# Optimization experiments

Hardware: AMD Instinct MI355X
Metric: run time of the kernel (lower is better)

Reference implementation:

```python
import jax, jax.numpy as jnp
import numpy as np

C = 768
H = 12
HD = C // H  # 64


def setup_inputs() -> dict:
    key = jax.random.key(0)
    k1, k2, k3, k4, k5, k6 = jax.random.split(key, 6)
    B, T = 8, 1024
    x = jax.random.normal(k1, (B, T, C), dtype=jnp.float32)
    mask = jax.random.randint(k2, (B, T), 0, 2, dtype=jnp.int32)
    # Linear params stored so that y = x @ W + b (W is [in, out])
    W_attn = jax.random.normal(k3, (C, 3 * C), dtype=jnp.float32) * 0.02
    b_attn = jax.random.normal(k4, (3 * C,), dtype=jnp.float32) * 0.02
    W_proj = jax.random.normal(k5, (C, C), dtype=jnp.float32) * 0.02
    b_proj = jax.random.normal(k6, (C,), dtype=jnp.float32) * 0.02
    return {"x": x, "mask": mask, "W_attn": W_attn, "b_attn": b_attn,
            "W_proj": W_proj, "b_proj": b_proj}


def reference(x, mask, W_attn, b_attn, W_proj, b_proj):
    B, T, _ = x.shape
    qkv = x @ W_attn + b_attn                      # [B, T, 3C]
    q, k, v = jnp.split(qkv, 3, axis=2)            # each [B, T, C]
    # [B, T, C] -> [B, H, T, HD]
    q = q.reshape(B, T, H, HD).transpose(0, 2, 1, 3)
    k = k.reshape(B, T, H, HD).transpose(0, 2, 1, 3)
    v = v.reshape(B, T, H, HD).transpose(0, 2, 1, 3)

    scale = 1.0 / np.sqrt(HD).astype(np.float32)
    att = jnp.einsum('bhqd,bhkd->bhqk', q, k) * scale  # [B, H, T, T]

    causal = jnp.tril(jnp.ones((T, T), dtype=bool))    # [T, T]
    att = jnp.where(causal[None, None], att, -jnp.inf)

    # custom mask: per-(batch, query-row) flag; where mask==0 the whole row
    # of scores is overwritten with 0.0001 (AFTER causal fill, as in torch)
    row_masked = (mask == 0)[:, None, :, None]         # [B, 1, T, 1]
    att = jnp.where(row_masked, jnp.float32(1e-4), att)

    att = jax.nn.softmax(att, axis=-1)
    # dropout layers are identity in eval mode
    y = jnp.einsum('bhqk,bhkd->bhqd', att, v)          # [B, H, T, HD]
    y = y.transpose(0, 2, 1, 3).reshape(B, T, C)
    y = y @ W_proj + b_proj
    return y
```

## Files before the change

kernel.cpp:

```cpp
#include <hip/hip_runtime.h>

#define BQ 8
#define TT 1024
#define CC 768
#define NH 12
#define HD 64
#define BH (BQ*NH)
#define MROWS (BQ*TT)
#define NQKV (3*CC)
#define KD CC

typedef unsigned short u16;
typedef __attribute__((ext_vector_type(4))) short short4v;
typedef __attribute__((ext_vector_type(8))) short short8v;
typedef __attribute__((ext_vector_type(4))) float floatx4;
typedef __attribute__((address_space(1))) const unsigned int gu32;
typedef __attribute__((address_space(3))) unsigned int lu32;

__device__ __forceinline__ float bf2f(u16 u) {
  union { unsigned int i; float f; } c; c.i = ((unsigned int)u) << 16; return c.f;
}
__device__ __forceinline__ u16 f2bf(float f) {
  union { float f; unsigned int i; } c; c.f = f;
  unsigned int i = c.i;
  return (u16)((i + 0x7FFFu + ((i >> 16) & 1u)) >> 16);
}
__device__ __forceinline__ float fast_exp2(float x) {
  return __builtin_amdgcn_exp2f(x);
}
__device__ __forceinline__ void async_ld16(const u16* g, u16* l) {
  __builtin_amdgcn_global_load_lds((gu32*)g, (lu32*)l, 16, 0, 0);
}

__global__ __launch_bounds__(256) void convert_f32_bf16(
    const float* __restrict__ in, u16* __restrict__ out, int n)
{
  int i = (blockIdx.x * 256 + threadIdx.x) * 4;
  if (i >= n) return;
  floatx4 v = *(const floatx4*)(in + i);
  short4v o;
  o[0] = (short)f2bf(v[0]); o[1] = (short)f2bf(v[1]);
  o[2] = (short)f2bf(v[2]); o[3] = (short)f2bf(v[3]);
  *(short4v*)(out + i) = o;
}

__global__ __launch_bounds__(256) void transpose_f32_bf16(
    const float* __restrict__ in, u16* __restrict__ out, int R, int Cc)
{
  __shared__ float tile[32][33];
  int ct = Cc >> 5;
  int bx = blockIdx.x % ct;
  int by = blockIdx.x / ct;
  int tx = threadIdx.x & 31;
  int ty = threadIdx.x >> 5;
  int c0 = bx << 5, r0 = by << 5;
#pragma unroll
  for (int s = 0; s < 4; ++s)
    tile[ty + s*8][tx] = in[(size_t)(r0 + ty + s*8) * Cc + c0 + tx];
  __syncthreads();
#pragma unroll
  for (int s = 0; s < 4; ++s)
    out[(size_t)(c0 + ty + s*8) * R + r0 + tx] = f2bf(tile[tx][ty + s*8]);
}

__global__ __launch_bounds__(256) void gemm_bt(
    const u16* __restrict__ A, const u16* __restrict__ Bt,
    const float* __restrict__ bias,
    float* __restrict__ out,
    u16* __restrict__ qo, u16* __restrict__ ko, u16* __restrict__ vo,
    int M, int N, int mode)
{
  __shared__ u16 As[64 * 64];
  __shared__ u16 Bs[128 * 64];

  int tid = threadIdx.x;
  int lane = tid & 63;
  int w = tid >> 6;
  int c = lane & 15;
  int q4 = lane >> 4;

  int mtiles = M >> 6;
  int mt = blockIdx.x % mtiles;
  int nt = blockIdx.x / mtiles;
  int m0 = mt << 6, n0 = nt << 7;

  int wr = (w >> 1) << 5;
  int wc = (w & 1) << 6;

  int srow8 = lane >> 3;
  int ug = ((lane & 7) ^ srow8) << 3;
  const u16* ag = A  + (size_t)(m0 + w * 16 + srow8) * KD + ug;
  const u16* bg = Bt + (size_t)(n0 + w * 32 + srow8) * KD + ug;
  u16* asl = &As[(w * 16) * 64];
  u16* bsl = &Bs[(w * 32) * 64];

  floatx4 acc[2][4];
#pragma unroll
  for (int mi = 0; mi < 2; ++mi)
#pragma unroll
    for (int ni = 0; ni < 4; ++ni) acc[mi][ni] = (floatx4){0.f, 0.f, 0.f, 0.f};

  int c7 = c & 7;

#pragma unroll 1
  for (int kt = 0; kt < KD; kt += 64) {
    async_ld16(ag + kt,              asl);
    async_ld16(ag + kt + 8 * KD,     asl + 8 * 64);
    async_ld16(bg + kt,              bsl);
    async_ld16(bg + kt + 8 * KD,     bsl + 8 * 64);
    async_ld16(bg + kt + 16 * KD,    bsl + 16 * 64);
    async_ld16(bg + kt + 24 * KD,    bsl + 24 * 64);
    __syncthreads();

    short8v af[2][2], bf[4][2];
#pragma unroll
    for (int kc = 0; kc < 2; ++kc) {
      int uoff = ((kc * 4 + q4) ^ c7) << 3;
#pragma unroll
      for (int mi = 0; mi < 2; ++mi)
        af[mi][kc] = *(const short8v*)&As[(wr + mi * 16 + c) * 64 + uoff];
#pragma unroll
      for (int ni = 0; ni < 4; ++ni)
        bf[ni][kc] = *(const short8v*)&Bs[(wc + ni * 16 + c) * 64 + uoff];
    }
#pragma unroll
    for (int kc = 0; kc < 2; ++kc)
#pragma unroll
      for (int mi = 0; mi < 2; ++mi)
#pragma unroll
        for (int ni = 0; ni < 4; ++ni)
          acc[mi][ni] = __builtin_amdgcn_mfma_f32_16x16x32_bf16(af[mi][kc], bf[ni][kc], acc[mi][ni], 0, 0, 0);
    __syncthreads();
  }

  if (mode == 0) {
    int which = (n0 + wc) / CC;
    int nbase = (n0 + wc) - which * CC;
    u16* dst0 = (which == 0) ? qo : ((which == 1) ? ko : vo);
#pragma unroll
    for (int ni = 0; ni < 4; ++ni) {
      int nn = nbase + ni * 16 + c;
      int hh = nn >> 6, dd = nn & 63;
      float bv = bias[which * CC + nn];
#pragma unroll
      for (int mi = 0; mi < 2; ++mi) {
#pragma unroll
        for (int r = 0; r < 4; ++r) {
          int mm = m0 + wr + mi * 16 + q4 * 4 + r;
          int bb = mm >> 10, tt = mm & 1023;
          size_t idx = (((size_t)(bb * NH + hh)) * TT + tt) * HD + dd;
          dst0[idx] = f2bf(acc[mi][ni][r] + bv);
        }
      }
    }
  } else {
#pragma unroll
    for (int ni = 0; ni < 4; ++ni) {
      int nn = n0 + wc + ni * 16 + c;
      float bv = bias[nn];
#pragma unroll
      for (int mi = 0; mi < 2; ++mi) {
#pragma unroll
        for (int r = 0; r < 4; ++r) {
          int mm = m0 + wr + mi * 16 + q4 * 4 + r;
          out[(size_t)mm * N + nn] = acc[mi][ni][r] + bv;
        }
      }
    }
  }
}

__global__ __launch_bounds__(256) void transpose_v(
    const u16* __restrict__ vb, u16* __restrict__ vt)
{
  __shared__ u16 tile[64][72];
  int tid = threadIdx.x;
  int tt0 = (blockIdx.x & 15) << 6;
  int bh = blockIdx.x >> 4;
  {
    int trow = tid >> 2;
    int dchunk = (tid & 3) << 4;
    const u16* src = vb + (((size_t)bh * TT + tt0 + trow) * HD) + dchunk;
    *(short8v*)&tile[trow][dchunk]     = *(const short8v*)src;
    *(short8v*)&tile[trow][dchunk + 8] = *(const short8v*)(src + 8);
  }
  __syncthreads();
  {
    int drow = tid >> 2;
    int tchunk = (tid & 3) << 4;
    short8v a, bv;
#pragma unroll
    for (int j = 0; j < 8; ++j) {
      a[j]  = (short)tile[tchunk + j][drow];
      bv[j] = (short)tile[tchunk + 8 + j][drow];
    }
    u16* dst = vt + ((size_t)bh * HD + drow) * TT + tt0 + tchunk;
    *(short8v*)dst       = a;
    *(short8v*)(dst + 8) = bv;
  }
}

__global__ __launch_bounds__(64) void vmean_kernel(
    const u16* __restrict__ vb, float* __restrict__ mv)
{
  int bh = blockIdx.x;
  int d = threadIdx.x;
  const u16* p = vb + (size_t)bh * TT * HD + d;
  float s0 = 0.f, s1 = 0.f, s2 = 0.f, s3 = 0.f;
  for (int t = 0; t < TT; t += 4) {
    s0 += bf2f(p[(size_t)(t + 0) * HD]);
    s1 += bf2f(p[(size_t)(t + 1) * HD]);
    s2 += bf2f(p[(size_t)(t + 2) * HD]);
    s3 += bf2f(p[(size_t)(t + 3) * HD]);
  }
  mv[bh * HD + d] = (s0 + s1 + s2 + s3) * (1.0f / 1024.0f);
}

__global__ __launch_bounds__(256) void knorm_kernel(
    const u16* __restrict__ kb, float* __restrict__ kmaxn)
{
  __shared__ float red[256];
  int bh = blockIdx.x;
  int tid = threadIdx.x;
  float mx = 0.f;
#pragma unroll 1
  for (int t = tid; t < TT; t += 256) {
    const u16* p = kb + ((size_t)bh * TT + t) * HD;
    float s = 0.f;
#pragma unroll
    for (int j = 0; j < 64; j += 8) {
      short8v v = *(const short8v*)(p + j);
#pragma unroll
      for (int i = 0; i < 8; ++i) {
        float f = bf2f((u16)v[i]);
        s = fmaf(f, f, s);
      }
    }
    mx = fmaxf(mx, s);
  }
  red[tid] = mx;
  __syncthreads();
  for (int s2 = 128; s2 > 0; s2 >>= 1) {
    if (tid < s2) red[tid] = fmaxf(red[tid], red[tid + s2]);
    __syncthreads();
  }
  if (tid == 0) kmaxn[bh] = sqrtf(red[0]);
}

#define LDW 72
#define SCL 0.18033688f

__global__ __launch_bounds__(256) void attn_kernel(
    const u16* __restrict__ qb, const u16* __restrict__ kb,
    const u16* __restrict__ vtb, const int* __restrict__ mask,
    const float* __restrict__ meanv, const float* __restrict__ kmaxn,
    u16* __restrict__ outb)
{
  __shared__ u16 Ks[64 * LDW];
  __shared__ u16 Vs[64 * LDW];
  __shared__ u16 Ps[4][16 * LDW];

  int tid = threadIdx.x;
  int lane = tid & 63;
  int w = tid >> 6;
  int c = lane & 15;
  int q4 = lane >> 4;

  int pair = blockIdx.x & 7;
  int bh = blockIdx.x >> 3;
  int b = bh / NH;
  int h = bh - b * NH;
  float kmax = kmaxn[bh];

  int srow = tid >> 2;
  int schunk = (tid & 3) << 4;
  const u16* kgp = kb + ((size_t)bh * TT + srow) * HD + schunk;
  const u16* vgp = vtb + ((size_t)bh * HD + srow) * TT + schunk;
  u16* ksw = &Ks[srow * LDW + schunk];
  u16* vsw = &Vs[srow * LDW + schunk];
  u16* pw = &Ps[w][0];

  short8v onesv;
#pragma unroll
  for (int j = 0; j < 8; ++j) onesv[j] = (short)0x3F80;

#pragma unroll 1
  for (int phase = 0; phase < 2; ++phase) {
    int qt = phase ? (15 - pair) : pair;
    int rowbase = (qt << 6) + (w << 4);

    short8v qfrag[2];
    {
      const u16* qp = qb + ((size_t)bh * TT + rowbase + c) * HD + q4 * 8;
      qfrag[0] = *(const short8v*)qp;
      qfrag[1] = *(const short8v*)(qp + 32);
    }

    float q2 = 0.f;
#pragma unroll
    for (int kc = 0; kc < 2; ++kc)
#pragma unroll
      for (int j = 0; j < 8; ++j) {
        float qv = bf2f((u16)qfrag[kc][j]);
        q2 = fmaf(qv, qv, q2);
      }
    q2 += __shfl_xor(q2, 16);
    q2 += __shfl_xor(q2, 32);
    float Mc = sqrtf(q2) * kmax * SCL;
    float Mrow[4];
#pragma unroll
    for (int r = 0; r < 4; ++r) Mrow[r] = __shfl(Mc, (q4 << 2) + r);

    floatx4 o[4];
#pragma unroll
    for (int i = 0; i < 4; ++i) o[i] = (floatx4){0.f, 0.f, 0.f, 0.f};
    floatx4 o5 = (floatx4){0.f, 0.f, 0.f, 0.f};

    short8v kr0, kr1, vr0, vr1;
    kr0 = *(const short8v*)kgp;
    kr1 = *(const short8v*)(kgp + 8);
    vr0 = *(const short8v*)vgp;
    vr1 = *(const short8v*)(vgp + 8);

#pragma unroll 1
    for (int kt = 0; kt <= qt; ++kt) {
      __syncthreads();
      *(short8v*)ksw = kr0; *(short8v*)(ksw + 8) = kr1;
      *(short8v*)vsw = vr0; *(short8v*)(vsw + 8) = vr1;
      __syncthreads();

      if (kt < qt) {
        const u16* kp = kgp + ((size_t)(kt + 1) << 6) * HD;
        const u16* vp = vgp + ((kt + 1) << 6);
        kr0 = *(const short8v*)kp;
        kr1 = *(const short8v*)(kp + 8);
        vr0 = *(const short8v*)vp;
        vr1 = *(const short8v*)(vp + 8);
      }

      floatx4 s[4];
#pragma unroll
      for (int nt = 0; nt < 4; ++nt) s[nt] = (floatx4){0.f, 0.f, 0.f, 0.f};
#pragma unroll
      for (int kc = 0; kc < 2; ++kc) {
#pragma unroll
        for (int nt = 0; nt < 4; ++nt) {
          short8v kf = *(const short8v*)&Ks[(nt * 16 + c) * LDW + kc * 32 + q4 * 8];
          s[nt] = __builtin_amdgcn_mfma_f32_16x16x32_bf16(qfrag[kc], kf, s[nt], 0, 0, 0);
        }
      }

      if (kt == qt) {
#pragma unroll
        for (int nt = 0; nt < 4; ++nt)
#pragma unroll
          for (int r = 0; r < 4; ++r) {
            float sv = s[nt][r];
            if (nt * 16 + c > (w << 4) + q4 * 4 + r) sv = -INFINITY;
            float p = fast_exp2(fmaf(sv, SCL, -Mrow[r]));
            pw[(q4 * 4 + r) * LDW + nt * 16 + c] = f2bf(p);
          }
      } else {
#pragma unroll
        for (int nt = 0; nt < 4; ++nt)
#pragma unroll
          for (int r = 0; r < 4; ++r) {
            float p = fast_exp2(fmaf(s[nt][r], SCL, -Mrow[r]));
            pw[(q4 * 4 + r) * LDW + nt * 16 + c] = f2bf(p);
          }
      }

#pragma unroll
      for (int kc = 0; kc < 2; ++kc) {
        short8v pf = *(const short8v*)&pw[c * LDW + kc * 32 + q4 * 8];
#pragma unroll
        for (int nt = 0; nt < 4; ++nt) {
          short8v vf = *(const short8v*)&Vs[(nt * 16 + c) * LDW + kc * 32 + q4 * 8];
          o[nt] = __builtin_amdgcn_mfma_f32_16x16x32_bf16(pf, vf, o[nt], 0, 0, 0);
        }
        o5 = __builtin_amdgcn_mfma_f32_16x16x32_bf16(pf, onesv, o5, 0, 0, 0);
      }
    }

    int qrow[4]; bool msk[4]; float inv[4];
#pragma unroll
    for (int r = 0; r < 4; ++r) {
      qrow[r] = rowbase + q4 * 4 + r;
      msk[r] = (mask[b * TT + qrow[r]] == 0);
      inv[r] = 1.f / o5[r];
    }
#pragma unroll
    for (int nt = 0; nt < 4; ++nt) {
      int d = nt * 16 + c;
      float mv = meanv[bh * HD + d];
#pragma unroll
      for (int r = 0; r < 4; ++r) {
        float val = msk[r] ? mv : o[nt][r] * inv[r];
        outb[((size_t)(b * TT + qrow[r])) * CC + h * HD + d] = f2bf(val);
      }
    }
  }
}

extern "C" void kernel_launch(void* const* d_in, const int* in_sizes, int n_in,
                              void* d_out, int out_size, void* d_ws, size_t ws_size,
                              hipStream_t stream)
{
  (void)in_sizes; (void)n_in; (void)out_size; (void)ws_size;
  const float* x     = (const float*)d_in[0];
  const int*   mask  = (const int*)d_in[1];
  const float* Wattn = (const float*)d_in[2];
  const float* battn = (const float*)d_in[3];
  const float* Wproj = (const float*)d_in[4];
  const float* bproj = (const float*)d_in[5];
  float* out = (float*)d_out;

  char* ws = (char*)d_ws;
  size_t off = 0;
  auto alloc = [&](size_t bytes) -> void* {
    void* p = ws + off;
    off += (bytes + 255) & ~(size_t)255;
    return p;
  };
  u16* WtA  = (u16*)alloc((size_t)NQKV * KD * 2);
  u16* WtP  = (u16*)alloc((size_t)CC * CC * 2);
  u16* xb   = (u16*)alloc((size_t)MROWS * CC * 2);
  u16* qbuf = (u16*)alloc((size_t)MROWS * CC * 2);
  u16* kbuf = (u16*)alloc((size_t)MROWS * CC * 2);
  u16* vbuf = (u16*)alloc((size_t)MROWS * CC * 2);
  u16* vtb  = (u16*)alloc((size_t)MROWS * CC * 2);
  u16* abuf = (u16*)alloc((size_t)MROWS * CC * 2);
  float* mv = (float*)alloc((size_t)BH * HD * 4);
  float* kmx = (float*)alloc((size_t)BH * 4);

  int nx = MROWS * CC;
  convert_f32_bf16<<<nx / (256 * 4), 256, 0, stream>>>(x, xb, nx);
  transpose_f32_bf16<<<(NQKV/32)*(KD/32), 256, 0, stream>>>(Wattn, WtA, KD, NQKV);
  transpose_f32_bf16<<<(CC/32)*(CC/32),   256, 0, stream>>>(Wproj, WtP, CC, CC);

  gemm_bt<<<(MROWS/64)*(NQKV/128), 256, 0, stream>>>(
      xb, WtA, battn, nullptr, qbuf, kbuf, vbuf, MROWS, NQKV, 0);

  transpose_v<<<BH * (TT/64), 256, 0, stream>>>(vbuf, vtb);
  vmean_kernel<<<BH, 64, 0, stream>>>(vbuf, mv);
  knorm_kernel<<<BH, 256, 0, stream>>>(kbuf, kmx);

  attn_kernel<<<BH * 8, 256, 0, stream>>>(qbuf, kbuf, vtb, mask, mv, kmx, abuf);

  gemm_bt<<<(MROWS/64)*(CC/128), 256, 0, stream>>>(
      abuf, WtP, bproj, out, nullptr, nullptr, nullptr, MROWS, CC, 1);
}
```

Before: 214.2 us.

## Fuse prep kernels, write V transposed from QKV GEMM, merge stats, transpose S MFMA

Merges the x conversion and the two weight transposes into one prep kernel. The QKV GEMM epilogue now writes V directly in [bh, d, t] layout, which removes the separate transpose_v pass and the vbuf buffer. The V-mean and K-norm kernels become one vk_stats kernel that reads the transposed V. In attention, the score MFMA operands are swapped so each lane holds one query row, which removes the per-row max shuffles and lets P be stored with 4-wide vector writes. The V store in the GEMM epilogue is now strided by T and may coalesce poorly.

```diff
diff --git a/kernel.cpp b/kernel.cpp
--- a/kernel.cpp
+++ b/kernel.cpp
@@ -32,27 +32,34 @@
   __builtin_amdgcn_global_load_lds((gu32*)g, (lu32*)l, 16, 0, 0);
 }
 
-__global__ __launch_bounds__(256) void convert_f32_bf16(
-    const float* __restrict__ in, u16* __restrict__ out, int n)
-{
-  int i = (blockIdx.x * 256 + threadIdx.x) * 4;
-  if (i >= n) return;
-  floatx4 v = *(const floatx4*)(in + i);
-  short4v o;
-  o[0] = (short)f2bf(v[0]); o[1] = (short)f2bf(v[1]);
-  o[2] = (short)f2bf(v[2]); o[3] = (short)f2bf(v[3]);
-  *(short4v*)(out + i) = o;
-}
-
-__global__ __launch_bounds__(256) void transpose_f32_bf16(
-    const float* __restrict__ in, u16* __restrict__ out, int R, int Cc)
+#define PREP_CONV 6144
+#define PREP_WA   1728
+
+__global__ __launch_bounds__(256) void prep_kernel(
+    const float* __restrict__ x, u16* __restrict__ xb,
+    const float* __restrict__ Wattn, u16* __restrict__ WtA,
+    const float* __restrict__ Wproj, u16* __restrict__ WtP)
 {
   __shared__ float tile[32][33];
+  int bid = blockIdx.x;
+  int tid = threadIdx.x;
+  if (bid < PREP_CONV) {
+    int i = (bid * 256 + tid) * 4;
+    floatx4 v = *(const floatx4*)(x + i);
+    short4v o;
+    o[0] = (short)f2bf(v[0]); o[1] = (short)f2bf(v[1]);
+    o[2] = (short)f2bf(v[2]); o[3] = (short)f2bf(v[3]);
+    *(short4v*)(xb + i) = o;
+    return;
+  }
+  const float* in; u16* out; int R, Cc, b2;
+  if (bid < PREP_CONV + PREP_WA) { in = Wattn; out = WtA; R = KD; Cc = NQKV; b2 = bid - PREP_CONV; }
+  else                           { in = Wproj; out = WtP; R = CC; Cc = CC;   b2 = bid - PREP_CONV - PREP_WA; }
   int ct = Cc >> 5;
-  int bx = blockIdx.x % ct;
-  int by = blockIdx.x / ct;
-  int tx = threadIdx.x & 31;
-  int ty = threadIdx.x >> 5;
+  int bx = b2 % ct;
+  int by = b2 / ct;
+  int tx = tid & 31;
+  int ty = tid >> 5;
   int c0 = bx << 5, r0 = by << 5;
 #pragma unroll
   for (int s = 0; s < 4; ++s)
@@ -148,7 +155,9 @@
         for (int r = 0; r < 4; ++r) {
           int mm = m0 + wr + mi * 16 + q4 * 4 + r;
           int bb = mm >> 10, tt = mm & 1023;
-          size_t idx = (((size_t)(bb * NH + hh)) * TT + tt) * HD + dd;
+          size_t bh = (size_t)(bb * NH + hh);
+          size_t idx = (which == 2) ? (bh * HD + dd) * TT + tt
+                                    : (bh * TT + tt) * HD + dd;
           dst0[idx] = f2bf(acc[mi][ni][r] + bv);
         }
       }
@@ -170,73 +179,46 @@
   }
 }
 
-__global__ __launch_bounds__(256) void transpose_v(
-    const u16* __restrict__ vb, u16* __restrict__ vt)
-{
-  __shared__ u16 tile[64][72];
-  int tid = threadIdx.x;
-  int tt0 = (blockIdx.x & 15) << 6;
-  int bh = blockIdx.x >> 4;
-  {
-    int trow = tid >> 2;
-    int dchunk = (tid & 3) << 4;
-    const u16* src = vb + (((size_t)bh * TT + tt0 + trow) * HD) + dchunk;
-    *(short8v*)&tile[trow][dchunk]     = *(const short8v*)src;
-    *(short8v*)&tile[trow][dchunk + 8] = *(const short8v*)(src + 8);
-  }
-  __syncthreads();
-  {
-    int drow = tid >> 2;
-    int tchunk = (tid & 3) << 4;
-    short8v a, bv;
-#pragma unroll
-    for (int j = 0; j < 8; ++j) {
-      a[j]  = (short)tile[tchunk + j][drow];
-      bv[j] = (short)tile[tchunk + 8 + j][drow];
-    }
-    u16* dst = vt + ((size_t)bh * HD + drow) * TT + tt0 + tchunk;
-    *(short8v*)dst       = a;
-    *(short8v*)(dst + 8) = bv;
-  }
-}
-
-__global__ __launch_bounds__(64) void vmean_kernel(
-    const u16* __restrict__ vb, float* __restrict__ mv)
-{
-  int bh = blockIdx.x;
-  int d = threadIdx.x;
-  const u16* p = vb + (size_t)bh * TT * HD + d;
-  float s0 = 0.f, s1 = 0.f, s2 = 0.f, s3 = 0.f;
-  for (int t = 0; t < TT; t += 4) {
-    s0 += bf2f(p[(size_t)(t + 0) * HD]);
-    s1 += bf2f(p[(size_t)(t + 1) * HD]);
-    s2 += bf2f(p[(size_t)(t + 2) * HD]);
-    s3 += bf2f(p[(size_t)(t + 3) * HD]);
-  }
-  mv[bh * HD + d] = (s0 + s1 + s2 + s3) * (1.0f / 1024.0f);
-}
-
-__global__ __launch_bounds__(256) void knorm_kernel(
-    const u16* __restrict__ kb, float* __restrict__ kmaxn)
+__global__ __launch_bounds__(256) void vk_stats(
+    const u16* __restrict__ vtb, const u16* __restrict__ kb,
+    float* __restrict__ mv, float* __restrict__ kmaxn)
 {
   __shared__ float red[256];
   int bh = blockIdx.x;
   int tid = threadIdx.x;
+  int d = tid & 63;
+  int g4 = tid >> 6;
+
+  {
+    const u16* vp = vtb + ((size_t)bh * HD + d) * TT + g4 * 256;
+    float s = 0.f;
+#pragma unroll 4
+    for (int j = 0; j < 256; j += 8) {
+      short8v v = *(const short8v*)(vp + j);
+#pragma unroll
+      for (int i = 0; i < 8; ++i) s += bf2f((u16)v[i]);
+    }
+    red[tid] = s;
+  }
+  __syncthreads();
+  if (g4 == 0) mv[bh * HD + d] = (red[d] + red[d + 64] + red[d + 128] + red[d + 192]) * (1.0f / 1024.0f);
+  __syncthreads();
+
   float mx = 0.f;
 #pragma unroll 1
   for (int t = tid; t < TT; t += 256) {
     const u16* p = kb + ((size_t)bh * TT + t) * HD;
-    float s = 0.f;
+    float ss = 0.f;
 #pragma unroll
     for (int j = 0; j < 64; j += 8) {
       short8v v = *(const short8v*)(p + j);
 #pragma unroll
       for (int i = 0; i < 8; ++i) {
         float f = bf2f((u16)v[i]);
-        s = fmaf(f, f, s);
-      }
-    }
-    mx = fmaxf(mx, s);
+        ss = fmaf(f, f, ss);
+      }
+    }
+    mx = fmaxf(mx, ss);
   }
   red[tid] = mx;
   __syncthreads();
@@ -307,9 +289,6 @@
     q2 += __shfl_xor(q2, 16);
     q2 += __shfl_xor(q2, 32);
     float Mc = sqrtf(q2) * kmax * SCL;
-    float Mrow[4];
-#pragma unroll
-    for (int r = 0; r < 4; ++r) Mrow[r] = __shfl(Mc, (q4 << 2) + r);
 
     floatx4 o[4];
 #pragma unroll
@@ -346,28 +325,21 @@
 #pragma unroll
         for (int nt = 0; nt < 4; ++nt) {
           short8v kf = *(const short8v*)&Ks[(nt * 16 + c) * LDW + kc * 32 + q4 * 8];
-          s[nt] = __builtin_amdgcn_mfma_f32_16x16x32_bf16(qfrag[kc], kf, s[nt], 0, 0, 0);
+          s[nt] = __builtin_amdgcn_mfma_f32_16x16x32_bf16(kf, qfrag[kc], s[nt], 0, 0, 0);
         }
       }
 
-      if (kt == qt) {
-#pragma unroll
-        for (int nt = 0; nt < 4; ++nt)
-#pragma unroll
-          for (int r = 0; r < 4; ++r) {
-            float sv = s[nt][r];
-            if (nt * 16 + c > (w << 4) + q4 * 4 + r) sv = -INFINITY;
-            float p = fast_exp2(fmaf(sv, SCL, -Mrow[r]));
-            pw[(q4 * 4 + r) * LDW + nt * 16 + c] = f2bf(p);
-          }
-      } else {
-#pragma unroll
-        for (int nt = 0; nt < 4; ++nt)
-#pragma unroll
-          for (int r = 0; r < 4; ++r) {
-            float p = fast_exp2(fmaf(s[nt][r], SCL, -Mrow[r]));
-            pw[(q4 * 4 + r) * LDW + nt * 16 + c] = f2bf(p);
-          }
+      int qrl = (w << 4) + c;
+#pragma unroll
+      for (int nt = 0; nt < 4; ++nt) {
+        short4v pk;
+#pragma unroll
+        for (int r = 0; r < 4; ++r) {
+          float sv = s[nt][r];
+          if (kt == qt && (nt * 16 + (q4 << 2) + r > qrl)) sv = -INFINITY;
+          pk[r] = (short)f2bf(fast_exp2(fmaf(sv, SCL, -Mc)));
+        }
+        *(short4v*)&pw[c * LDW + nt * 16 + (q4 << 2)] = pk;
       }
 
 #pragma unroll
@@ -427,23 +399,17 @@
   u16* xb   = (u16*)alloc((size_t)MROWS * CC * 2);
   u16* qbuf = (u16*)alloc((size_t)MROWS * CC * 2);
   u16* kbuf = (u16*)alloc((size_t)MROWS * CC * 2);
-  u16* vbuf = (u16*)alloc((size_t)MROWS * CC * 2);
   u16* vtb  = (u16*)alloc((size_t)MROWS * CC * 2);
   u16* abuf = (u16*)alloc((size_t)MROWS * CC * 2);
   float* mv = (float*)alloc((size_t)BH * HD * 4);
   float* kmx = (float*)alloc((size_t)BH * 4);
 
-  int nx = MROWS * CC;
-  convert_f32_bf16<<<nx / (256 * 4), 256, 0, stream>>>(x, xb, nx);
-  transpose_f32_bf16<<<(NQKV/32)*(KD/32), 256, 0, stream>>>(Wattn, WtA, KD, NQKV);
-  transpose_f32_bf16<<<(CC/32)*(CC/32),   256, 0, stream>>>(Wproj, WtP, CC, CC);
+  prep_kernel<<<8448, 256, 0, stream>>>(x, xb, Wattn, WtA, Wproj, WtP);
 
   gemm_bt<<<(MROWS/64)*(NQKV/128), 256, 0, stream>>>(
-      xb, WtA, battn, nullptr, qbuf, kbuf, vbuf, MROWS, NQKV, 0);
-
-  transpose_v<<<BH * (TT/64), 256, 0, stream>>>(vbuf, vtb);
-  vmean_kernel<<<BH, 64, 0, stream>>>(vbuf, mv);
-  knorm_kernel<<<BH, 256, 0, stream>>>(kbuf, kmx);
+      xb, WtA, battn, nullptr, qbuf, kbuf, vtb, MROWS, NQKV, 0);
+
+  vk_stats<<<BH, 256, 0, stream>>>(vtb, kbuf, mv, kmx);
 
   attn_kernel<<<BH * 8, 256, 0, stream>>>(qbuf, kbuf, vtb, mask, mv, kmx, abuf);
 
```

Result: no change. 211.4 us (-1.3%).
